# Performance work log

Measured on AMD Instinct MI355X. Metric: run time of the kernel, lower is better.

Reference implementation:

```python
import jax, jax.numpy as jnp
import numpy as np

BETA = 0.25      # commitment loss weight
DECAY = 0.99     # EMA decay
EPS = 1e-5       # Laplace smoothing for counts


def setup_inputs() -> dict:
    key = jax.random.key(0)
    k1, k2, k3 = jax.random.split(key, 3)
    B, d, h, w, K = 16, 64, 64, 64, 1024
    z_e = jax.random.normal(k1, (B, d, h, w), dtype=jnp.float32)
    codebook = jax.random.normal(k2, (K, d), dtype=jnp.float32)
    ema_count = jnp.ones((K,), dtype=jnp.float32)
    ema_sum = jax.random.normal(k3, (K, d), dtype=jnp.float32)
    return {"z_e": z_e, "codebook": codebook, "ema_count": ema_count, "ema_sum": ema_sum}


def reference(z_e, codebook, ema_count, ema_sum):
    B, d, h, w = z_e.shape
    K = codebook.shape[0]
    # [B,d,h,w] -> [N,d], N = B*h*w
    z_flat = jnp.transpose(z_e, (0, 2, 3, 1)).reshape(-1, d)
    # squared euclidean distances [N,K]
    dist = (jnp.sum(z_flat * z_flat, axis=1, keepdims=True)
            - 2.0 * (z_flat @ codebook.T)
            + jnp.sum(codebook * codebook, axis=1)[None, :])
    indices = jnp.argmin(dist, axis=1)                      # [N] int
    e_k = codebook[indices].reshape(B, h, w, d).transpose(0, 3, 1, 2)  # [B,d,h,w]

    # --- EMA codebook update (training mode, no grad) ---
    zf = jax.lax.stop_gradient(z_flat)
    counts = jax.ops.segment_sum(jnp.ones((zf.shape[0],), dtype=zf.dtype), indices, num_segments=K)
    sums = jax.ops.segment_sum(zf, indices, num_segments=K)
    new_count = ema_count * DECAY + (1.0 - DECAY) * counts
    new_sum = ema_sum * DECAY + (1.0 - DECAY) * sums
    n = jnp.sum(new_count)
    count_s = (new_count + EPS) / (n + K * EPS) * n
    new_codebook = new_sum / count_s[:, None]

    # straight-through estimator
    e_k_ste = z_e + jax.lax.stop_gradient(e_k - z_e)
    L_commit = (jnp.mean((z_e - jax.lax.stop_gradient(e_k)) ** 2)
                + BETA * jnp.mean((jax.lax.stop_gradient(z_e) - e_k) ** 2))
    return (e_k_ste, indices.reshape(B, h, w), L_commit, new_codebook, new_count, new_sum)
```

## Files before the change

### kernel.cpp

```cpp
#include <hip/hip_runtime.h>
#include <hip/hip_bf16.h>
#include <hip/hip_fp16.h>

#define NB 16
#define DD 64
#define HW 4096
#define NTOT 65536
#define KC 1024

#define O_EK   0
#define O_IDX  4194304
#define O_L    4259840
#define O_CB   4259841
#define O_CNT  4325377
#define O_SUM  4326401

#define WS_IDX    0
#define WS_LCPART 65536
#define WS_N      66048
#define WS_CNORM  66560
#define WS_PSUM   67584
#define WS_PCNT   329728
#define WS_FLGC   333824
#define WS_FLGL   334336
#define WS_CBH    399360
#define WS_CBL    432128

#define MARGIN 0.002f
#define MAXFLG 32

typedef _Float16 v8h __attribute__((ext_vector_type(8)));
typedef float    v4f __attribute__((ext_vector_type(4)));

__global__ __launch_bounds__(256) void k_pre(const float* __restrict__ cb,
                                             const float* __restrict__ ema_count,
                                             float* __restrict__ cnorm,
                                             float* __restrict__ n_ws,
                                             unsigned short* __restrict__ cbh,
                                             unsigned short* __restrict__ cbl) {
    const int t = threadIdx.x;
    const int w = (blockIdx.x * 256 + t) >> 6;
    const int l = t & 63;
    float s = 0.f;
    if (l < 16) {
        float4 v = *(const float4*)(cb + (size_t)w * DD + l * 4);
        s = v.x * v.x + v.y * v.y + v.z * v.z + v.w * v.w;
    }
#pragma unroll
    for (int m = 1; m <= 8; m <<= 1) s += __shfl_xor(s, m, 64);
    if (l == 0) cnorm[w] = s;

    const int e4 = blockIdx.x * 256 + t;
    if (e4 < 16384) {
        float4 v4 = ((const float4*)cb)[e4];
        __half hx = __float2half(v4.x), hy = __float2half(v4.y),
               hz = __float2half(v4.z), hw2 = __float2half(v4.w);
        ushort4 h4 = { __half_as_ushort(hx), __half_as_ushort(hy),
                       __half_as_ushort(hz), __half_as_ushort(hw2) };
        ((ushort4*)cbh)[e4] = h4;
        ushort4 l4 = { __half_as_ushort(__float2half(v4.x - __half2float(hx))),
                       __half_as_ushort(__float2half(v4.y - __half2float(hy))),
                       __half_as_ushort(__float2half(v4.z - __half2float(hz))),
                       __half_as_ushort(__float2half(v4.w - __half2float(hw2))) };
        ((ushort4*)cbl)[e4] = l4;
    }

    if (blockIdx.x == 0) {
        __shared__ float red[256];
        red[t] = ema_count[t] + ema_count[t + 256] + ema_count[t + 512] + ema_count[t + 768];
        __syncthreads();
        for (int s2 = 128; s2 >= 1; s2 >>= 1) {
            if (t < s2) red[t] += red[t + s2];
            __syncthreads();
        }
        if (t == 0) n_ws[0] = 0.99f * red[0] + 0.01f * 65536.0f;
    }
}

__global__ __launch_bounds__(256) void k_argmin(const float* __restrict__ z_e,
                                                const unsigned short* __restrict__ cbh,
                                                const unsigned short* __restrict__ cbl,
                                                const float* __restrict__ cnorm,
                                                int* __restrict__ idx_ws,
                                                int* __restrict__ flg_cnt,
                                                int* __restrict__ flg_list,
                                                float* __restrict__ out) {
    __shared__ __align__(16) unsigned short A2h[8][128][8];
    __shared__ __align__(16) unsigned short A2l[8][128][8];
    __shared__ __align__(16) unsigned short B2h[2][8][64][8];
    __shared__ __align__(16) unsigned short B2l[2][8][64][8];
    __shared__ int idx_lds[128];
    __shared__ int flagrows[128];
    __shared__ int nflag;

    float* slab = (float*)&B2h[0][0][0][0];

    const int t  = threadIdx.x;
    const int n0 = blockIdx.x * 128;
    const int b   = n0 >> 12;
    const int hw0 = n0 & 4095;
    const float* zbase = z_e + (size_t)b * (DD * HW) + hw0;

    if (t == 0) nflag = 0;

    for (int sl = 0; sl < 2; ++sl) {
        if (sl) __syncthreads();
#pragma unroll
        for (int s = 0; s < 4; ++s) {
            int idx = t + s * 256;
            int j   = idx >> 5;
            int m4  = (idx & 31) << 2;
            float4 v = *(const float4*)(zbase + (size_t)(sl * 32 + j) * HW + m4);
            *(float4*)&slab[j * 128 + m4] = v;
        }
        __syncthreads();
#pragma unroll
        for (int s = 0; s < 2; ++s) {
            int ss  = t + s * 256;
            int chl = ss >> 7;
            int m   = ss & 127;
            int ch  = sl * 4 + chl;
            unsigned hv[4], lv[4];
#pragma unroll
            for (int p = 0; p < 4; ++p) {
                float v0 = slab[(chl * 8 + 2 * p    ) * 128 + m];
                float v1 = slab[(chl * 8 + 2 * p + 1) * 128 + m];
                __half h0 = __float2half(v0), h1 = __float2half(v1);
                __half l0 = __float2half(v0 - __half2float(h0));
                __half l1 = __float2half(v1 - __half2float(h1));
                hv[p] = (unsigned)__half_as_ushort(h0) | ((unsigned)__half_as_ushort(h1) << 16);
                lv[p] = (unsigned)__half_as_ushort(l0) | ((unsigned)__half_as_ushort(l1) << 16);
            }
            uint4 hq = {hv[0], hv[1], hv[2], hv[3]};
            uint4 lq = {lv[0], lv[1], lv[2], lv[3]};
            *(uint4*)&A2h[ch][m][0] = hq;
            *(uint4*)&A2l[ch][m][0] = lq;
        }
    }
    __syncthreads();

    const int w    = t >> 6;
    const int lane = t & 63;
    const int c    = lane & 15;
    const int q    = lane >> 4;

    const int ch0   = t >> 6;
    const int code0 = t & 63;
    const int ch1   = 4 + (t >> 6);
    const int code1 = t & 63;

    v8h Afh[2][2], Afl[2][2];
#pragma unroll
    for (int g = 0; g < 2; ++g) {
        int m = 32 * w + 16 * g + c;
#pragma unroll
        for (int s = 0; s < 2; ++s) {
            Afh[g][s] = *(const v8h*)&A2h[s * 4 + q][m][0];
            Afl[g][s] = *(const v8h*)&A2l[s * 4 + q][m][0];
        }
    }

    {
        size_t g0 = ((size_t)code0) * 64 + ch0 * 8;
        size_t g1 = ((size_t)code1) * 64 + ch1 * 8;
        *(uint4*)&B2h[0][ch0][code0][0] = *(const uint4*)(cbh + g0);
        *(uint4*)&B2l[0][ch0][code0][0] = *(const uint4*)(cbl + g0);
        *(uint4*)&B2h[0][ch1][code1][0] = *(const uint4*)(cbh + g1);
        *(uint4*)&B2l[0][ch1][code1][0] = *(const uint4*)(cbl + g1);
    }
    __syncthreads();

    float m1v[2][4], m2v[2][4]; int m1i[2][4];
#pragma unroll
    for (int g = 0; g < 2; ++g)
#pragma unroll
        for (int r = 0; r < 4; ++r) { m1v[g][r] = 3.4e38f; m2v[g][r] = 3.4e38f; m1i[g][r] = 0; }

    for (int kt = 0; kt < 16; ++kt) {
        const int cur = kt & 1, nxt = cur ^ 1;
        uint4 ph0, pl0, ph1, pl1;
        if (kt < 15) {
            size_t g0 = ((size_t)((kt + 1) * 64 + code0)) * 64 + ch0 * 8;
            size_t g1 = ((size_t)((kt + 1) * 64 + code1)) * 64 + ch1 * 8;
            ph0 = *(const uint4*)(cbh + g0);
            pl0 = *(const uint4*)(cbl + g0);
            ph1 = *(const uint4*)(cbh + g1);
            pl1 = *(const uint4*)(cbl + g1);
        }

#pragma unroll
        for (int sub = 0; sub < 4; ++sub) {
            const int cl = sub * 16 + c;
            v8h Bfh0 = *(const v8h*)&B2h[cur][q][cl][0];
            v8h Bfh1 = *(const v8h*)&B2h[cur][4 + q][cl][0];
            v8h Bfl0 = *(const v8h*)&B2l[cur][q][cl][0];
            v8h Bfl1 = *(const v8h*)&B2l[cur][4 + q][cl][0];
            const int kg = kt * 64 + cl;
            float cnc = cnorm[kg];
#pragma unroll
            for (int g = 0; g < 2; ++g) {
                v4f acc = {0.f, 0.f, 0.f, 0.f};
                acc = __builtin_amdgcn_mfma_f32_16x16x32_f16(Afh[g][0], Bfh0, acc, 0, 0, 0);
                acc = __builtin_amdgcn_mfma_f32_16x16x32_f16(Afh[g][1], Bfh1, acc, 0, 0, 0);
                acc = __builtin_amdgcn_mfma_f32_16x16x32_f16(Afh[g][0], Bfl0, acc, 0, 0, 0);
                acc = __builtin_amdgcn_mfma_f32_16x16x32_f16(Afh[g][1], Bfl1, acc, 0, 0, 0);
                acc = __builtin_amdgcn_mfma_f32_16x16x32_f16(Afl[g][0], Bfh0, acc, 0, 0, 0);
                acc = __builtin_amdgcn_mfma_f32_16x16x32_f16(Afl[g][1], Bfh1, acc, 0, 0, 0);
#pragma unroll
                for (int r = 0; r < 4; ++r) {
                    float v = fmaf(-2.0f, acc[r], cnc);
                    bool better = v < m1v[g][r];
                    m2v[g][r] = better ? m1v[g][r] : fminf(m2v[g][r], v);
                    m1i[g][r] = better ? kg : m1i[g][r];
                    m1v[g][r] = better ? v : m1v[g][r];
                }
            }
        }

        if (kt < 15) {
            *(uint4*)&B2h[nxt][ch0][code0][0] = ph0;
            *(uint4*)&B2l[nxt][ch0][code0][0] = pl0;
            *(uint4*)&B2h[nxt][ch1][code1][0] = ph1;
            *(uint4*)&B2l[nxt][ch1][code1][0] = pl1;
        }
        __syncthreads();
    }

#pragma unroll
    for (int g = 0; g < 2; ++g)
#pragma unroll
        for (int r = 0; r < 4; ++r) {
            float a = m1v[g][r], b2 = m2v[g][r]; int ii = m1i[g][r];
#pragma unroll
            for (int mask = 1; mask <= 8; mask <<= 1) {
                float ov = __shfl_xor(a, mask, 64);
                int   oi = __shfl_xor(ii, mask, 64);
                float o2 = __shfl_xor(b2, mask, 64);
                bool take = (ov < a) || (ov == a && oi < ii);
                float loser = take ? a : ov;
                b2 = fminf(fminf(b2, o2), loser);
                a  = take ? ov : a;
                ii = take ? oi : ii;
            }
            if (c == 0) {
                int row = 32 * w + 16 * g + q * 4 + r;
                idx_lds[row] = ii;
                if ((b2 - a) < MARGIN) { int p = atomicAdd(&nflag, 1); flagrows[p] = row; }
            }
        }
    __syncthreads();

    int nf = nflag; if (nf > MAXFLG) nf = MAXFLG;
    if (t == 0) flg_cnt[blockIdx.x] = nf;
    if (t < nf) flg_list[blockIdx.x * MAXFLG + t] = flagrows[t];

    if (t < 128) {
        int bi = idx_lds[t];
        out[O_IDX + n0 + t] = (float)bi;
        idx_ws[n0 + t] = bi;
    }
}

__global__ __launch_bounds__(256) void k_fix(const float* __restrict__ z_e,
                                             const float* __restrict__ cb,
                                             const float* __restrict__ cnorm,
                                             const int* __restrict__ flg_cnt,
                                             const int* __restrict__ flg_list,
                                             int* __restrict__ idx_ws,
                                             float* __restrict__ out) {
    const int blk = blockIdx.x;
    const int nf = flg_cnt[blk];
    if (nf == 0) return;
    __shared__ float redv4[4];
    __shared__ int   redi4[4];
    const int t = threadIdx.x;
    const int lane = t & 63, w = t >> 6;
    const int n0 = blk * 128;
    const int b   = n0 >> 12;
    const int hw0 = n0 & 4095;

    for (int f = 0; f < nf; ++f) {
        int row = flg_list[blk * MAXFLG + f];
        const float* zrow = z_e + (size_t)b * (DD * HW) + hw0 + row;
        float znr = 0.f;
        for (int j = 0; j < 64; ++j) { float v = zrow[(size_t)j * HW]; znr = fmaf(v, v, znr); }
        float best = 3.4e38f; int bi = 0;
#pragma unroll
        for (int c2 = 0; c2 < 4; ++c2) {
            int k = t * 4 + c2;
            const float* ck = cb + (size_t)k * DD;
            float acc = 0.f;
            for (int j = 0; j < 64; ++j) acc = fmaf(zrow[(size_t)j * HW], ck[j], acc);
            float v = (znr - 2.0f * acc) + cnorm[k];
            if (v < best) { best = v; bi = k; }
        }
#pragma unroll
        for (int mask = 1; mask <= 32; mask <<= 1) {
            float ov = __shfl_xor(best, mask, 64);
            int   oi = __shfl_xor(bi, mask, 64);
            if (ov < best || (ov == best && oi < bi)) { best = ov; bi = oi; }
        }
        if (lane == 0) { redv4[w] = best; redi4[w] = bi; }
        __syncthreads();
        if (t == 0) {
            float bv = redv4[0]; int bix = redi4[0];
#pragma unroll
            for (int w2 = 1; w2 < 4; ++w2)
                if (redv4[w2] < bv || (redv4[w2] == bv && redi4[w2] < bix)) { bv = redv4[w2]; bix = redi4[w2]; }
            idx_ws[n0 + row] = bix;
            out[O_IDX + n0 + row] = (float)bix;
        }
        __syncthreads();
    }
}

__global__ __launch_bounds__(1024) void k_out(const int* __restrict__ idx_ws,
                                              const float* __restrict__ z_e,
                                              const float* __restrict__ cb,
                                              float* __restrict__ psum,
                                              int* __restrict__ pcnt,
                                              float* __restrict__ lc_part,
                                              float* __restrict__ out) {
    __shared__ float acc[KC];
    __shared__ int bins[KC];
    __shared__ float cbj[KC];
    __shared__ float lcr[16];
    const int j = blockIdx.x & 63;
    const int c = blockIdx.x >> 6;
    const int t = threadIdx.x;
    acc[t] = 0.f;
    bins[t] = 0;
    cbj[t] = cb[(size_t)t * DD + j];
    __syncthreads();
    const float* zj = z_e + (size_t)j * HW;
    float* oj = out + O_EK + (size_t)j * HW;
    const int base = c * 16384;
    float lc = 0.f;
#pragma unroll
    for (int i = 0; i < 4; ++i) {
        int n4 = base + i * 4096 + t * 4;
        int b = n4 >> 12, hw = n4 & 4095;
        size_t zoff = (size_t)b * (DD * HW) + hw;
        float4 z4 = *(const float4*)(zj + zoff);
        int4   k4 = *(const int4*)(idx_ws + n4);
        float e0 = cbj[k4.x], e1 = cbj[k4.y], e2 = cbj[k4.z], e3 = cbj[k4.w];
        float4 o4 = { z4.x + (e0 - z4.x), z4.y + (e1 - z4.y),
                      z4.z + (e2 - z4.z), z4.w + (e3 - z4.w) };
        *(float4*)(oj + zoff) = o4;
        float d0 = z4.x - e0, d1 = z4.y - e1, d2 = z4.z - e2, d3 = z4.w - e3;
        lc = fmaf(d0, d0, lc); lc = fmaf(d1, d1, lc);
        lc = fmaf(d2, d2, lc); lc = fmaf(d3, d3, lc);
        atomicAdd(&acc[k4.x], z4.x);
        atomicAdd(&acc[k4.y], z4.y);
        atomicAdd(&acc[k4.z], z4.z);
        atomicAdd(&acc[k4.w], z4.w);
        if (j == 0) {
            atomicAdd(&bins[k4.x], 1); atomicAdd(&bins[k4.y], 1);
            atomicAdd(&bins[k4.z], 1); atomicAdd(&bins[k4.w], 1);
        }
    }
    __syncthreads();
    psum[(size_t)c * 65536 + j * 1024 + t] = acc[t];
    if (j == 0) pcnt[c * 1024 + t] = bins[t];
#pragma unroll
    for (int m = 32; m >= 1; m >>= 1) lc += __shfl_xor(lc, m, 64);
    if ((t & 63) == 0) lcr[t >> 6] = lc;
    __syncthreads();
    if (t == 0) {
        float s = 0.f;
#pragma unroll
        for (int u = 0; u < 16; ++u) s += lcr[u];
        lc_part[blockIdx.x] = s;
    }
}

__global__ __launch_bounds__(1024) void k_epi(const float* __restrict__ psum,
                                              const int* __restrict__ pcnt,
                                              const float* __restrict__ ema_sum,
                                              const float* __restrict__ ema_count,
                                              const float* __restrict__ n_ws,
                                              const float* __restrict__ lc_part,
                                              float* __restrict__ out) {
    const int t = threadIdx.x;
    const int e = blockIdx.x * 1024 + t;
    const int k = e >> 6, j = e & 63;
    float s4 = psum[j * 1024 + k] + psum[65536 + j * 1024 + k]
             + psum[131072 + j * 1024 + k] + psum[196608 + j * 1024 + k];
    float ns = ema_sum[e] * 0.99f + 0.01f * s4;
    out[O_SUM + e] = ns;
    int cnt = pcnt[k] + pcnt[1024 + k] + pcnt[2048 + k] + pcnt[3072 + k];
    float nc = ema_count[k] * 0.99f + 0.01f * (float)cnt;
    float n  = n_ws[0];
    float cs = (nc + 1e-5f) / (n + 1024.0f * 1e-5f) * n;
    out[O_CB + e] = ns / cs;
    if (blockIdx.x == 0) {
        int c2 = pcnt[t] + pcnt[1024 + t] + pcnt[2048 + t] + pcnt[3072 + t];
        out[O_CNT + t] = ema_count[t] * 0.99f + 0.01f * (float)c2;
    }
    if (blockIdx.x == 1) {
        __shared__ float red[512];
        if (t < 512) red[t] = (t < 256) ? lc_part[t] : 0.f;
        __syncthreads();
        for (int s = 256; s >= 1; s >>= 1) {
            if (t < s) red[t] += red[t + s];
            __syncthreads();
        }
        if (t == 0) out[O_L] = 1.25f * red[0] * (1.0f / 4194304.0f);
    }
}

extern "C" void kernel_launch(void* const* d_in, const int* in_sizes, int n_in,
                              void* d_out, int out_size, void* d_ws, size_t ws_size,
                              hipStream_t stream) {
    const float* z_e       = (const float*)d_in[0];
    const float* cb        = (const float*)d_in[1];
    const float* ema_count = (const float*)d_in[2];
    const float* ema_sum   = (const float*)d_in[3];
    float* out             = (float*)d_out;

    float* ws_f      = (float*)d_ws;
    int*   idx_ws    = (int*)d_ws;
    float* lc_part   = ws_f + WS_LCPART;
    float* n_ws      = ws_f + WS_N;
    float* cnorm_ws  = ws_f + WS_CNORM;
    float* psum      = ws_f + WS_PSUM;
    int*   pcnt      = (int*)(ws_f + WS_PCNT);
    int*   flg_cnt   = (int*)(ws_f + WS_FLGC);
    int*   flg_list  = (int*)(ws_f + WS_FLGL);
    unsigned short* cbh = (unsigned short*)(ws_f + WS_CBH);
    unsigned short* cbl = (unsigned short*)(ws_f + WS_CBL);

    k_pre<<<256, 256, 0, stream>>>(cb, ema_count, cnorm_ws, n_ws, cbh, cbl);
    k_argmin<<<NTOT / 128, 256, 0, stream>>>(z_e, cbh, cbl, cnorm_ws, idx_ws, flg_cnt, flg_list, out);
    k_fix<<<NTOT / 128, 256, 0, stream>>>(z_e, cb, cnorm_ws, flg_cnt, flg_list, idx_ws, out);
    k_out<<<256, 1024, 0, stream>>>(idx_ws, z_e, cb, psum, pcnt, lc_part, out);
    k_epi<<<64, 1024, 0, stream>>>(psum, pcnt, ema_sum, ema_count, n_ws, lc_part, out);
}
```

Before: 159.5 us.

## Fuse near-tie refinement into argmin kernel using tracked top-2 candidates

The argmin kernel now tracks the second-best code index as well as its value, and re-checks flagged near-tie rows in fp32 directly, comparing only the top two candidates. This removes the separate k_fix launch, which rescanned all 1024 codes per flagged row, along with its global flag lists. The cost is more registers and select instructions in the inner loop, plus a correctness risk: the true nearest code may fall outside the fp16-split top two. The per-block flag cap of 32 is also gone.

```diff
diff --git a/kernel.cpp b/kernel.cpp
--- a/kernel.cpp
+++ b/kernel.cpp
@@ -21,13 +21,10 @@
 #define WS_CNORM  66560
 #define WS_PSUM   67584
 #define WS_PCNT   329728
-#define WS_FLGC   333824
-#define WS_FLGL   334336
 #define WS_CBH    399360
 #define WS_CBL    432128
 
 #define MARGIN 0.002f
-#define MAXFLG 32
 
 typedef _Float16 v8h __attribute__((ext_vector_type(8)));
 typedef float    v4f __attribute__((ext_vector_type(4)));
@@ -78,12 +75,11 @@
 }
 
 __global__ __launch_bounds__(256) void k_argmin(const float* __restrict__ z_e,
+                                                const float* __restrict__ cbf,
                                                 const unsigned short* __restrict__ cbh,
                                                 const unsigned short* __restrict__ cbl,
                                                 const float* __restrict__ cnorm,
                                                 int* __restrict__ idx_ws,
-                                                int* __restrict__ flg_cnt,
-                                                int* __restrict__ flg_list,
                                                 float* __restrict__ out) {
     __shared__ __align__(16) unsigned short A2h[8][128][8];
     __shared__ __align__(16) unsigned short A2l[8][128][8];
@@ -91,6 +87,8 @@
     __shared__ __align__(16) unsigned short B2l[2][8][64][8];
     __shared__ int idx_lds[128];
     __shared__ int flagrows[128];
+    __shared__ int flagi1[128];
+    __shared__ int flagi2[128];
     __shared__ int nflag;
 
     float* slab = (float*)&B2h[0][0][0][0];
@@ -170,11 +168,14 @@
     }
     __syncthreads();
 
-    float m1v[2][4], m2v[2][4]; int m1i[2][4];
+    float m1v[2][4], m2v[2][4]; int m1i[2][4], m2i[2][4];
 #pragma unroll
     for (int g = 0; g < 2; ++g)
 #pragma unroll
-        for (int r = 0; r < 4; ++r) { m1v[g][r] = 3.4e38f; m2v[g][r] = 3.4e38f; m1i[g][r] = 0; }
+        for (int r = 0; r < 4; ++r) {
+            m1v[g][r] = 3.4e38f; m2v[g][r] = 3.4e38f;
+            m1i[g][r] = 0;       m2i[g][r] = 0;
+        }
 
     for (int kt = 0; kt < 16; ++kt) {
         const int cur = kt & 1, nxt = cur ^ 1;
@@ -209,10 +210,14 @@
 #pragma unroll
                 for (int r = 0; r < 4; ++r) {
                     float v = fmaf(-2.0f, acc[r], cnc);
-                    bool better = v < m1v[g][r];
-                    m2v[g][r] = better ? m1v[g][r] : fminf(m2v[g][r], v);
-                    m1i[g][r] = better ? kg : m1i[g][r];
-                    m1v[g][r] = better ? v : m1v[g][r];
+                    bool b1 = v < m1v[g][r];
+                    bool bs = v < m2v[g][r];
+                    float nm2v = b1 ? m1v[g][r] : (bs ? v  : m2v[g][r]);
+                    int   nm2i = b1 ? m1i[g][r] : (bs ? kg : m2i[g][r]);
+                    m1i[g][r] = b1 ? kg : m1i[g][r];
+                    m1v[g][r] = b1 ? v  : m1v[g][r];
+                    m2v[g][r] = nm2v;
+                    m2i[g][r] = nm2i;
                 }
             }
         }
@@ -230,87 +235,63 @@
     for (int g = 0; g < 2; ++g)
 #pragma unroll
         for (int r = 0; r < 4; ++r) {
-            float a = m1v[g][r], b2 = m2v[g][r]; int ii = m1i[g][r];
+            float a = m1v[g][r];  int ii = m1i[g][r];
+            float b2 = m2v[g][r]; int i2 = m2i[g][r];
 #pragma unroll
             for (int mask = 1; mask <= 8; mask <<= 1) {
-                float ov = __shfl_xor(a, mask, 64);
-                int   oi = __shfl_xor(ii, mask, 64);
-                float o2 = __shfl_xor(b2, mask, 64);
-                bool take = (ov < a) || (ov == a && oi < ii);
-                float loser = take ? a : ov;
-                b2 = fminf(fminf(b2, o2), loser);
-                a  = take ? ov : a;
+                float o1  = __shfl_xor(a,  mask, 64);
+                int   oi  = __shfl_xor(ii, mask, 64);
+                float o2  = __shfl_xor(b2, mask, 64);
+                int   o2i = __shfl_xor(i2, mask, 64);
+                bool take = (o1 < a) || (o1 == a && oi < ii);
+                float loserV = take ? a  : o1;
+                int   loserI = take ? ii : oi;
+                bool c2 = (o2 < b2);
+                float cv = c2 ? o2  : b2;
+                int   ci = c2 ? o2i : i2;
+                bool l2 = (loserV < cv);
+                b2 = l2 ? loserV : cv;
+                i2 = l2 ? loserI : ci;
+                a  = take ? o1 : a;
                 ii = take ? oi : ii;
             }
             if (c == 0) {
                 int row = 32 * w + 16 * g + q * 4 + r;
                 idx_lds[row] = ii;
-                if ((b2 - a) < MARGIN) { int p = atomicAdd(&nflag, 1); flagrows[p] = row; }
-            }
-        }
-    __syncthreads();
-
-    int nf = nflag; if (nf > MAXFLG) nf = MAXFLG;
-    if (t == 0) flg_cnt[blockIdx.x] = nf;
-    if (t < nf) flg_list[blockIdx.x * MAXFLG + t] = flagrows[t];
+                if ((b2 - a) < MARGIN) {
+                    int p = atomicAdd(&nflag, 1);
+                    flagrows[p] = row; flagi1[p] = ii; flagi2[p] = i2;
+                }
+            }
+        }
+    __syncthreads();
+
+    {
+        int nf = nflag;
+        for (int f = w; f < nf; f += 4) {
+            int row = flagrows[f], i1 = flagi1[f], i2x = flagi2[f];
+            const float* zrow = z_e + (size_t)b * (DD * HW) + hw0 + row;
+            float zj = zrow[(size_t)lane * HW];
+            float p1 = zj * cbf[(size_t)i1  * DD + lane];
+            float p2 = zj * cbf[(size_t)i2x * DD + lane];
+#pragma unroll
+            for (int mask = 1; mask <= 32; mask <<= 1) {
+                p1 += __shfl_xor(p1, mask, 64);
+                p2 += __shfl_xor(p2, mask, 64);
+            }
+            if (lane == 0) {
+                float d1 = fmaf(-2.0f, p1, cnorm[i1]);
+                float d2 = fmaf(-2.0f, p2, cnorm[i2x]);
+                if (d2 < d1 || (d2 == d1 && i2x < i1)) idx_lds[row] = i2x;
+            }
+        }
+    }
+    __syncthreads();
 
     if (t < 128) {
         int bi = idx_lds[t];
         out[O_IDX + n0 + t] = (float)bi;
         idx_ws[n0 + t] = bi;
-    }
-}
-
-__global__ __launch_bounds__(256) void k_fix(const float* __restrict__ z_e,
-                                             const float* __restrict__ cb,
-                                             const float* __restrict__ cnorm,
-                                             const int* __restrict__ flg_cnt,
-                                             const int* __restrict__ flg_list,
-                                             int* __restrict__ idx_ws,
-                                             float* __restrict__ out) {
-    const int blk = blockIdx.x;
-    const int nf = flg_cnt[blk];
-    if (nf == 0) return;
-    __shared__ float redv4[4];
-    __shared__ int   redi4[4];
-    const int t = threadIdx.x;
-    const int lane = t & 63, w = t >> 6;
-    const int n0 = blk * 128;
-    const int b   = n0 >> 12;
-    const int hw0 = n0 & 4095;
-
-    for (int f = 0; f < nf; ++f) {
-        int row = flg_list[blk * MAXFLG + f];
-        const float* zrow = z_e + (size_t)b * (DD * HW) + hw0 + row;
-        float znr = 0.f;
-        for (int j = 0; j < 64; ++j) { float v = zrow[(size_t)j * HW]; znr = fmaf(v, v, znr); }
-        float best = 3.4e38f; int bi = 0;
-#pragma unroll
-        for (int c2 = 0; c2 < 4; ++c2) {
-            int k = t * 4 + c2;
-            const float* ck = cb + (size_t)k * DD;
-            float acc = 0.f;
-            for (int j = 0; j < 64; ++j) acc = fmaf(zrow[(size_t)j * HW], ck[j], acc);
-            float v = (znr - 2.0f * acc) + cnorm[k];
-            if (v < best) { best = v; bi = k; }
-        }
-#pragma unroll
-        for (int mask = 1; mask <= 32; mask <<= 1) {
-            float ov = __shfl_xor(best, mask, 64);
-            int   oi = __shfl_xor(bi, mask, 64);
-            if (ov < best || (ov == best && oi < bi)) { best = ov; bi = oi; }
-        }
-        if (lane == 0) { redv4[w] = best; redi4[w] = bi; }
-        __syncthreads();
-        if (t == 0) {
-            float bv = redv4[0]; int bix = redi4[0];
-#pragma unroll
-            for (int w2 = 1; w2 < 4; ++w2)
-                if (redv4[w2] < bv || (redv4[w2] == bv && redi4[w2] < bix)) { bv = redv4[w2]; bix = redi4[w2]; }
-            idx_ws[n0 + row] = bix;
-            out[O_IDX + n0 + row] = (float)bix;
-        }
-        __syncthreads();
     }
 }
 
@@ -425,14 +406,11 @@
     float* cnorm_ws  = ws_f + WS_CNORM;
     float* psum      = ws_f + WS_PSUM;
     int*   pcnt      = (int*)(ws_f + WS_PCNT);
-    int*   flg_cnt   = (int*)(ws_f + WS_FLGC);
-    int*   flg_list  = (int*)(ws_f + WS_FLGL);
     unsigned short* cbh = (unsigned short*)(ws_f + WS_CBH);
     unsigned short* cbl = (unsigned short*)(ws_f + WS_CBL);
 
     k_pre<<<256, 256, 0, stream>>>(cb, ema_count, cnorm_ws, n_ws, cbh, cbl);
-    k_argmin<<<NTOT / 128, 256, 0, stream>>>(z_e, cbh, cbl, cnorm_ws, idx_ws, flg_cnt, flg_list, out);
-    k_fix<<<NTOT / 128, 256, 0, stream>>>(z_e, cb, cnorm_ws, flg_cnt, flg_list, idx_ws, out);
+    k_argmin<<<NTOT / 128, 256, 0, stream>>>(z_e, cb, cbh, cbl, cnorm_ws, idx_ws, out);
     k_out<<<256, 1024, 0, stream>>>(idx_ws, z_e, cb, psum, pcnt, lc_part, out);
     k_epi<<<64, 1024, 0, stream>>>(psum, pcnt, ema_sum, ema_count, n_ws, lc_part, out);
 }
```

Measured after the change: 146.4 us. -8.2%, faster.
